# Kernel tuning notes

Measured on AMD Instinct MI355X. Metric: run time of the kernel, lower is better.

## Reference

```python
import jax, jax.numpy as jnp
import numpy as np

D = 1024
H = 16
K = D // H
B = 2
S = 2048

def setup_inputs() -> dict:
    key = jax.random.key(0)
    k1, k2, k3, k4, k5 = jax.random.split(key, 5)
    x = jax.random.normal(k1, (B, S, D), dtype=jnp.float32)
    # nn.Linear(d, 3d): weight [3d, d], bias [3d]
    Wqkv = jax.random.normal(k2, (3 * D, D), dtype=jnp.float32) / np.sqrt(D)
    bqkv = jax.random.normal(k3, (3 * D,), dtype=jnp.float32) * 0.01
    Wproj = jax.random.normal(k4, (D, D), dtype=jnp.float32) / np.sqrt(D)
    bproj = jax.random.normal(k5, (D,), dtype=jnp.float32) * 0.01
    return {"x": x, "Wqkv": Wqkv, "bqkv": bqkv, "Wproj": Wproj, "bproj": bproj}

def reference(x, Wqkv, bqkv, Wproj, bproj):
    Bsz, Slen, d = x.shape
    # fused QKV projection: [B,S,3d] -> [B,S,3,H,K] -> (3, B, H, S, K)
    qkv = (jnp.einsum('bsd,ed->bse', x, Wqkv) + bqkv).reshape(Bsz, Slen, 3, H, K)
    q, k, v = jnp.moveaxis(qkv, 2, 0).transpose(0, 1, 3, 2, 4)
    scale = 1.0 / jnp.sqrt(jnp.asarray(K, dtype=x.dtype))
    scores = jnp.einsum('bhqk,bhmk->bhqm', q, k) * scale  # [B,H,S,S]
    a = jax.nn.softmax(scores, axis=-1)
    # dropout is identity in eval mode
    o = jnp.einsum('bhqm,bhmk->bhqk', a, v)  # [B,H,S,K]
    o = o.transpose(0, 2, 1, 3).reshape(Bsz, Slen, d)
    return jnp.einsum('bsd,ed->bse', o, Wproj) + bproj
```

## Files before the change

kernel.cpp:

```cpp
#include <hip/hip_runtime.h>
#include <cstdint>

typedef unsigned short ushort_t;
typedef short short8 __attribute__((ext_vector_type(8)));
typedef float f32x4 __attribute__((ext_vector_type(4)));
typedef float float4v __attribute__((ext_vector_type(4)));
typedef unsigned int uint2v __attribute__((ext_vector_type(2)));

#define DDIM 1024
#define HH 16
#define HEADK 64
#define BB 2
#define SS 2048

#if __has_builtin(__builtin_amdgcn_exp2f)
#define EXP2F(x) __builtin_amdgcn_exp2f(x)
#else
#define EXP2F(x) exp2f(x)
#endif

__device__ __forceinline__ ushort_t f2bf(float f) {
  union { float f; uint32_t u; } c; c.f = f;
  uint32_t u = c.u;
  u += 0x7fffu + ((u >> 16) & 1u);
  return (ushort_t)(u >> 16);
}

__device__ __forceinline__ uint32_t pkbf_trunc(float a, float b) {
  union { float f; uint32_t u; } ca, cb;
  ca.f = a; cb.f = b;
  return __builtin_amdgcn_perm(cb.u, ca.u, 0x07060302);
}

__device__ __forceinline__ uint32_t pkbf_rne(float a, float b) {
  return (uint32_t)f2bf(a) | ((uint32_t)f2bf(b) << 16);
}

__device__ __forceinline__ void glds16(const ushort_t* gp, ushort_t* lp) {
  __builtin_amdgcn_global_load_lds(
      (const __attribute__((address_space(1))) uint32_t*)gp,
      (__attribute__((address_space(3))) uint32_t*)lp, 16, 0, 0);
}

__global__ void cvt3_kernel(const float* __restrict__ s0, ushort_t* __restrict__ d0, int n0,
                            const float* __restrict__ s1, ushort_t* __restrict__ d1, int n1,
                            const float* __restrict__ s2, ushort_t* __restrict__ d2, int n2) {
  int i = blockIdx.x * blockDim.x + threadIdx.x;
  const float* src; ushort_t* dst; int k;
  if (i < n0) { src = s0; dst = d0; k = i; }
  else if (i < n0 + n1) { src = s1; dst = d1; k = i - n0; }
  else if (i < n0 + n1 + n2) { src = s2; dst = d2; k = i - n0 - n1; }
  else return;
  float4v v = ((const float4v*)src)[k];
  uint2v o; o[0] = pkbf_rne(v[0], v[1]); o[1] = pkbf_rne(v[2], v[3]);
  ((uint2v*)dst)[k] = o;
}

template <int MODE, int TM>
__global__ __launch_bounds__(256) void gemm_nt(
    const ushort_t* __restrict__ A, const ushort_t* __restrict__ Bm,
    const float* __restrict__ bias, float* __restrict__ Cout,
    ushort_t* __restrict__ Cbf, int M, int N, int Kd) {
  __shared__ ushort_t smem[128 * 64 * 2];
  ushort_t* As = smem;
  ushort_t* Bs = smem + TM * 64;
  const int MI = TM / 32;
  const int tid = threadIdx.x;
  const int wv = tid >> 6, lane = tid & 63;
  const int l15 = lane & 15, quad = lane >> 4;
  const int wm = wv >> 1, wn = wv & 1;
  const int tm0 = blockIdx.y * TM, tn0 = blockIdx.x * 128;

  f32x4 acc[MI][4];
#pragma unroll
  for (int i = 0; i < MI; ++i)
#pragma unroll
    for (int j = 0; j < 4; ++j) acc[i][j] = (f32x4){0.f, 0.f, 0.f, 0.f};

  const int lrow = lane >> 3;
  const int gcb = (lane & 7) ^ lrow;
  const int ACI = TM / 32;

  for (int k0 = 0; k0 < Kd; k0 += 64) {
#pragma unroll
    for (int c = 0; c < ACI; ++c) {
      int seg = wv * ACI + c;
      glds16(A + (size_t)(tm0 + seg * 8 + lrow) * Kd + k0 + gcb * 8,
             As + seg * 512);
    }
#pragma unroll
    for (int c = 0; c < 4; ++c) {
      int seg = wv * 4 + c;
      glds16(Bm + (size_t)(tn0 + seg * 8 + lrow) * Kd + k0 + gcb * 8,
             Bs + seg * 512);
    }
    __syncthreads();
#pragma unroll
    for (int kk = 0; kk < 64; kk += 32) {
      short8 af[MI], bfr[4];
#pragma unroll
      for (int i = 0; i < MI; ++i) {
        int r = wm * (TM / 2) + i * 16 + l15;
        int cb = (kk >> 3) + quad;
        af[i] = *(const short8*)(As + r * 64 + ((cb ^ (l15 & 7)) << 3));
      }
#pragma unroll
      for (int j = 0; j < 4; ++j) {
        int r = wn * 64 + j * 16 + l15;
        int cb = (kk >> 3) + quad;
        bfr[j] = *(const short8*)(Bs + r * 64 + ((cb ^ (l15 & 7)) << 3));
      }
#pragma unroll
      for (int i = 0; i < MI; ++i)
#pragma unroll
        for (int j = 0; j < 4; ++j)
          acc[i][j] = __builtin_amdgcn_mfma_f32_16x16x32_bf16(
              af[i], bfr[j], acc[i][j], 0, 0, 0);
    }
    __syncthreads();
  }

  if (MODE == 1) {
#pragma unroll
    for (int j = 0; j < 4; ++j) {
      int col = tn0 + wn * 64 + j * 16 + l15;
      float bv = bias[col];
#pragma unroll
      for (int i = 0; i < MI; ++i) {
        int row0 = tm0 + wm * (TM / 2) + i * 16 + quad * 4;
#pragma unroll
        for (int r = 0; r < 4; ++r)
          Cout[(size_t)(row0 + r) * N + col] = acc[i][j][r] + bv;
      }
    }
  } else {
    const int t = tn0 >> 10;
    if (t < 2) {
#pragma unroll
      for (int j = 0; j < 4; ++j) {
        int col = tn0 + wn * 64 + j * 16 + l15;
        float bv = bias[col];
        int hh = (col >> 6) & 15, kk2 = col & 63;
#pragma unroll
        for (int i = 0; i < MI; ++i) {
          int row0 = tm0 + wm * (TM / 2) + i * 16 + quad * 4;
#pragma unroll
          for (int r = 0; r < 4; ++r) {
            int row = row0 + r;
            int b = row >> 11, s = row & 2047;
            float v = acc[i][j][r] + bv;
            if (t == 0) v *= 0.18033688f;
            size_t base =
                (((size_t)t * BB + b) * HH + hh) * ((size_t)SS * HEADK);
            Cbf[base + (size_t)s * HEADK + kk2] = f2bf(v);
          }
        }
      }
    } else {
      __syncthreads();
#pragma unroll
      for (int j = 0; j < 4; ++j) {
        int c = wn * 64 + j * 16 + l15;
        float bv = bias[tn0 + c];
#pragma unroll
        for (int i = 0; i < MI; ++i) {
          int row0 = wm * (TM / 2) + i * 16 + quad * 4;
          uint2v dw;
          dw[0] = pkbf_rne(acc[i][j][0] + bv, acc[i][j][1] + bv);
          dw[1] = pkbf_rne(acc[i][j][2] + bv, acc[i][j][3] + bv);
          int rb = row0 >> 3;
          *(uint2v*)(&smem[c * 128 + (((rb ^ (c & 15)) << 3) | (row0 & 7))]) =
              dw;
        }
      }
      __syncthreads();
      const int rb2 = lane & 15;
      const int cg = lane >> 4;
#pragma unroll
      for (int it = 0; it < 8; ++it) {
        int c = wv * 32 + it * 4 + cg;
        short8 vv = *(const short8*)(&smem[c * 128 + ((rb2 ^ (c & 15)) << 3)]);
        int gcol = tn0 + c;
        int hh = (gcol >> 6) & 15, kk2 = gcol & 63;
        int grow = tm0 + rb2 * 8;
        int b = grow >> 11, s = grow & 2047;
        size_t base = (((size_t)2 * BB + b) * HH + hh) * ((size_t)SS * HEADK);
        *(short8*)(&Cbf[base + (size_t)kk2 * SS + s]) = vv;
      }
    }
  }
}

__global__ __launch_bounds__(256, 2) void attn_kernel(
    const ushort_t* __restrict__ qkv, ushort_t* __restrict__ ob) {
  __shared__ ushort_t Kt[2][64 * 64];
  __shared__ ushort_t Vt[2][64 * 64];
  __shared__ ushort_t Pw[4][32 * 64];

  const int qt = blockIdx.x, h = blockIdx.y, b = blockIdx.z;
  const int tid = threadIdx.x;
  const int wv = tid >> 6, lane = tid & 63;
  const int l15 = lane & 15, quad = lane >> 4;

  const size_t hstride = (size_t)SS * HEADK;
  const ushort_t* Qg = qkv + ((size_t)(0 * BB + b) * HH + h) * hstride;
  const ushort_t* Kg = qkv + ((size_t)(1 * BB + b) * HH + h) * hstride;
  const ushort_t* Vg = qkv + ((size_t)(2 * BB + b) * HH + h) * hstride;

  short8 qf[2][2];
#pragma unroll
  for (int mi = 0; mi < 2; ++mi)
#pragma unroll
    for (int kc = 0; kc < 2; ++kc)
      qf[mi][kc] = *(const short8*)(
          Qg + (size_t)(qt * 128 + wv * 32 + mi * 16 + l15) * 64 + kc * 32 +
          quad * 8);

  const short ONE = (short)0x3F80;
  short8 ones = {ONE, ONE, ONE, ONE, ONE, ONE, ONE, ONE};

  f32x4 oat[2][4];
  f32x4 loa[2];
#pragma unroll
  for (int mi = 0; mi < 2; ++mi) {
    loa[mi] = (f32x4){0.f, 0.f, 0.f, 0.f};
#pragma unroll
    for (int c = 0; c < 4; ++c) oat[mi][c] = (f32x4){0.f, 0.f, 0.f, 0.f};
  }

  const int lrow = lane >> 3, gcb = (lane & 7) ^ lrow;

  auto stage = [&](int jj, int db) {
#pragma unroll
    for (int c = 0; c < 2; ++c) {
      int seg = wv * 2 + c;
      glds16(Kg + (size_t)(jj * 64 + seg * 8 + lrow) * 64 + gcb * 8,
             &Kt[db][seg * 512]);
    }
#pragma unroll
    for (int c = 0; c < 2; ++c) {
      int seg = wv * 2 + c;
      glds16(Vg + (size_t)(seg * 8 + lrow) * SS + jj * 64 + gcb * 8,
             &Vt[db][seg * 512]);
    }
  };

  stage(0, 0);

  for (int j = 0; j < 32; ++j) {
    const int db = j & 1;
    __syncthreads();
    if (j + 1 < 32) stage(j + 1, db ^ 1);

    f32x4 st[2][4];
#pragma unroll
    for (int cf = 0; cf < 4; ++cf) {
      int n = cf * 16 + l15;
      short8 kf0 = *(const short8*)(&Kt[db][n * 64 + ((quad ^ (n & 7)) << 3)]);
      short8 kf1 =
          *(const short8*)(&Kt[db][n * 64 + (((quad + 4) ^ (n & 7)) << 3)]);
#pragma unroll
      for (int mi = 0; mi < 2; ++mi) {
        f32x4 z = (f32x4){0.f, 0.f, 0.f, 0.f};
        z = __builtin_amdgcn_mfma_f32_16x16x32_bf16(kf0, qf[mi][0], z, 0, 0, 0);
        z = __builtin_amdgcn_mfma_f32_16x16x32_bf16(kf1, qf[mi][1], z, 0, 0, 0);
        st[mi][cf] = z;
      }
    }

#pragma unroll
    for (int mi = 0; mi < 2; ++mi)
#pragma unroll
      for (int cf = 0; cf < 4; ++cf) {
        float e0 = EXP2F(st[mi][cf][0]);
        float e1 = EXP2F(st[mi][cf][1]);
        float e2 = EXP2F(st[mi][cf][2]);
        float e3 = EXP2F(st[mi][cf][3]);
        uint2v dw;
        dw[0] = pkbf_trunc(e0, e1);
        dw[1] = pkbf_trunc(e2, e3);
        int row = mi * 16 + l15;
        int bb = 2 * cf + (quad >> 1);
        *(uint2v*)(&Pw[wv][row * 64 + ((bb ^ (l15 & 7)) << 3) +
                           (quad & 1) * 4]) = dw;
      }

    short8 pa[2][2];
#pragma unroll
    for (int mi = 0; mi < 2; ++mi)
#pragma unroll
      for (int kc = 0; kc < 2; ++kc)
        pa[mi][kc] = *(const short8*)(&Pw[wv][(mi * 16 + l15) * 64 +
                                              (((kc * 4 + quad) ^ (l15 & 7))
                                               << 3)]);

#pragma unroll
    for (int cf = 0; cf < 4; ++cf) {
      int f = cf * 16 + l15;
      short8 vb0 = *(const short8*)(&Vt[db][f * 64 + ((quad ^ (f & 7)) << 3)]);
      short8 vb1 =
          *(const short8*)(&Vt[db][f * 64 + (((quad + 4) ^ (f & 7)) << 3)]);
#pragma unroll
      for (int mi = 0; mi < 2; ++mi) {
        oat[mi][cf] = __builtin_amdgcn_mfma_f32_16x16x32_bf16(
            vb0, pa[mi][0], oat[mi][cf], 0, 0, 0);
        oat[mi][cf] = __builtin_amdgcn_mfma_f32_16x16x32_bf16(
            vb1, pa[mi][1], oat[mi][cf], 0, 0, 0);
      }
    }
#pragma unroll
    for (int mi = 0; mi < 2; ++mi) {
      loa[mi] = __builtin_amdgcn_mfma_f32_16x16x32_bf16(ones, pa[mi][0],
                                                        loa[mi], 0, 0, 0);
      loa[mi] = __builtin_amdgcn_mfma_f32_16x16x32_bf16(ones, pa[mi][1],
                                                        loa[mi], 0, 0, 0);
    }
  }

#pragma unroll
  for (int mi = 0; mi < 2; ++mi) {
    float inv = 1.0f / loa[mi][0];
#pragma unroll
    for (int cf = 0; cf < 4; ++cf) {
      uint2v dw;
      dw[0] = pkbf_rne(oat[mi][cf][0] * inv, oat[mi][cf][1] * inv);
      dw[1] = pkbf_rne(oat[mi][cf][2] * inv, oat[mi][cf][3] * inv);
      int row = mi * 16 + l15;
      int bb = 2 * cf + (quad >> 1);
      *(uint2v*)(&Pw[wv][row * 64 + ((bb ^ (l15 & 7)) << 3) + (quad & 1) * 4]) =
          dw;
    }
  }
  const int rr = lane >> 1, half = lane & 1;
#pragma unroll
  for (int c = 0; c < 4; ++c) {
    short8 ov = *(const short8*)(&Pw[wv][rr * 64 +
                                         (((half * 4 + c) ^ (rr & 7)) << 3)]);
    int row = qt * 128 + wv * 32 + rr;
    *(short8*)(&ob[(size_t)(b * SS + row) * DDIM + h * 64 + half * 32 +
                   c * 8]) = ov;
  }
}

extern "C" void kernel_launch(void* const* d_in, const int* in_sizes, int n_in,
                              void* d_out, int out_size, void* d_ws,
                              size_t ws_size, hipStream_t stream) {
  const float* x = (const float*)d_in[0];
  const float* Wqkv = (const float*)d_in[1];
  const float* bqkv = (const float*)d_in[2];
  const float* Wproj = (const float*)d_in[3];
  const float* bproj = (const float*)d_in[4];
  float* out = (float*)d_out;

  ushort_t* xb = (ushort_t*)d_ws;
  ushort_t* wqb = xb + (size_t)4096 * 1024;
  ushort_t* wpb = wqb + (size_t)3072 * 1024;
  ushort_t* qkvb = wpb + (size_t)1024 * 1024;
  ushort_t* obuf = qkvb + (size_t)3 * BB * HH * SS * HEADK;

  const int n0 = 4096 * 1024 / 4, n1 = 3072 * 1024 / 4, n2 = 1024 * 1024 / 4;
  cvt3_kernel<<<(n0 + n1 + n2 + 255) / 256, 256, 0, stream>>>(
      x, xb, n0, Wqkv, wqb, n1, Wproj, wpb, n2);
  gemm_nt<0, 128><<<dim3(3072 / 128, 4096 / 128), 256, 0, stream>>>(
      xb, wqb, bqkv, nullptr, qkvb, 4096, 3072, 1024);
  attn_kernel<<<dim3(SS / 128, HH, BB), 256, 0, stream>>>(qkvb, obuf);
  gemm_nt<1, 64><<<dim3(1024 / 128, 4096 / 64), 256, 0, stream>>>(
      obuf, wpb, bproj, out, nullptr, 4096, 1024, 1024);
}
```

Baseline: 193.1 us.

## Split attention over key halves with partial outputs and a reduce kernel

The attention kernel now splits the key sequence into two halves, each block processing 32-key tiles for one half. Unnormalized partial outputs (bf16) and partial row sums are written to aliased workspace buffers. A new reduce kernel sums the halves, normalizes, and writes the head-interleaved output. This doubles the block count and raises occupancy to increase parallelism across CUs, at the cost of extra global traffic, an extra launch, and an added bf16 rounding of the partials.

```diff
diff --git a/kernel.cpp b/kernel.cpp
--- a/kernel.cpp
+++ b/kernel.cpp
@@ -34,6 +34,13 @@
 
 __device__ __forceinline__ uint32_t pkbf_rne(float a, float b) {
   return (uint32_t)f2bf(a) | ((uint32_t)f2bf(b) << 16);
+}
+
+__device__ __forceinline__ float bfhi2f(uint32_t u) {
+  union { uint32_t u; float f; } c; c.u = u & 0xffff0000u; return c.f;
+}
+__device__ __forceinline__ float bflo2f(uint32_t u) {
+  union { uint32_t u; float f; } c; c.u = u << 16; return c.f;
 }
 
 __device__ __forceinline__ void glds16(const ushort_t* gp, ushort_t* lp) {
@@ -191,13 +198,15 @@
   }
 }
 
-__global__ __launch_bounds__(256, 2) void attn_kernel(
-    const ushort_t* __restrict__ qkv, ushort_t* __restrict__ ob) {
-  __shared__ ushort_t Kt[2][64 * 64];
-  __shared__ ushort_t Vt[2][64 * 64];
-  __shared__ ushort_t Pw[4][32 * 64];
-
-  const int qt = blockIdx.x, h = blockIdx.y, b = blockIdx.z;
+__global__ __launch_bounds__(256, 4) void attn_kernel(
+    const ushort_t* __restrict__ qkv, ushort_t* __restrict__ Op0,
+    ushort_t* __restrict__ Op1, float* __restrict__ Lp) {
+  __shared__ ushort_t Kt[2][32 * 64];
+  __shared__ ushort_t Vt[2][64 * 32];
+  __shared__ ushort_t Pw[4][32 * 32];
+
+  const int qt = blockIdx.x, h = blockIdx.y;
+  const int b = blockIdx.z >> 1, ns = blockIdx.z & 1;
   const int tid = threadIdx.x;
   const int wv = tid >> 6, lane = tid & 63;
   const int l15 = lane & 15, quad = lane >> 4;
@@ -206,6 +215,7 @@
   const ushort_t* Qg = qkv + ((size_t)(0 * BB + b) * HH + h) * hstride;
   const ushort_t* Kg = qkv + ((size_t)(1 * BB + b) * HH + h) * hstride;
   const ushort_t* Vg = qkv + ((size_t)(2 * BB + b) * HH + h) * hstride;
+  ushort_t* Opp = ns ? Op1 : Op0;
 
   short8 qf[2][2];
 #pragma unroll
@@ -229,20 +239,16 @@
   }
 
   const int lrow = lane >> 3, gcb = (lane & 7) ^ lrow;
+  const int vfl = lane >> 2;
+  const int vgb = (lane & 3) ^ ((vfl >> 1) & 3);
+
+  const int pos0 = ns * (SS / 2);
 
   auto stage = [&](int jj, int db) {
-#pragma unroll
-    for (int c = 0; c < 2; ++c) {
-      int seg = wv * 2 + c;
-      glds16(Kg + (size_t)(jj * 64 + seg * 8 + lrow) * 64 + gcb * 8,
-             &Kt[db][seg * 512]);
-    }
-#pragma unroll
-    for (int c = 0; c < 2; ++c) {
-      int seg = wv * 2 + c;
-      glds16(Vg + (size_t)(seg * 8 + lrow) * SS + jj * 64 + gcb * 8,
-             &Vt[db][seg * 512]);
-    }
+    glds16(Kg + (size_t)(pos0 + jj * 32 + wv * 8 + lrow) * 64 + gcb * 8,
+           &Kt[db][wv * 512]);
+    glds16(Vg + (size_t)(wv * 16 + vfl) * SS + pos0 + jj * 32 + vgb * 8,
+           &Vt[db][wv * 512]);
   };
 
   stage(0, 0);
@@ -252,9 +258,9 @@
     __syncthreads();
     if (j + 1 < 32) stage(j + 1, db ^ 1);
 
-    f32x4 st[2][4];
-#pragma unroll
-    for (int cf = 0; cf < 4; ++cf) {
+    f32x4 st[2][2];
+#pragma unroll
+    for (int cf = 0; cf < 2; ++cf) {
       int n = cf * 16 + l15;
       short8 kf0 = *(const short8*)(&Kt[db][n * 64 + ((quad ^ (n & 7)) << 3)]);
       short8 kf1 =
@@ -271,7 +277,7 @@
 #pragma unroll
     for (int mi = 0; mi < 2; ++mi)
 #pragma unroll
-      for (int cf = 0; cf < 4; ++cf) {
+      for (int cf = 0; cf < 2; ++cf) {
         float e0 = EXP2F(st[mi][cf][0]);
         float e1 = EXP2F(st[mi][cf][1]);
         float e2 = EXP2F(st[mi][cf][2]);
@@ -280,66 +286,90 @@
         dw[0] = pkbf_trunc(e0, e1);
         dw[1] = pkbf_trunc(e2, e3);
         int row = mi * 16 + l15;
-        int bb = 2 * cf + (quad >> 1);
-        *(uint2v*)(&Pw[wv][row * 64 + ((bb ^ (l15 & 7)) << 3) +
-                           (quad & 1) * 4]) = dw;
-      }
-
-    short8 pa[2][2];
+        int pb = 2 * cf + (quad >> 1);
+        int pbs = pb ^ ((l15 >> 1) & 3);
+        *(uint2v*)(&Pw[wv][row * 32 + pbs * 8 + (quad & 1) * 4]) = dw;
+      }
+
+    short8 pa[2];
+#pragma unroll
+    for (int mi = 0; mi < 2; ++mi) {
+      int row = mi * 16 + l15;
+      pa[mi] = *(const short8*)(&Pw[wv][row * 32 +
+                                        ((quad ^ ((l15 >> 1) & 3)) << 3)]);
+    }
+
+#pragma unroll
+    for (int cf = 0; cf < 4; ++cf) {
+      short8 vf = *(const short8*)(&Vt[db][(cf * 16 + l15) * 32 +
+                                           ((quad ^ ((l15 >> 1) & 3)) << 3)]);
+#pragma unroll
+      for (int mi = 0; mi < 2; ++mi)
+        oat[mi][cf] = __builtin_amdgcn_mfma_f32_16x16x32_bf16(
+            vf, pa[mi], oat[mi][cf], 0, 0, 0);
+    }
 #pragma unroll
     for (int mi = 0; mi < 2; ++mi)
-#pragma unroll
-      for (int kc = 0; kc < 2; ++kc)
-        pa[mi][kc] = *(const short8*)(&Pw[wv][(mi * 16 + l15) * 64 +
-                                              (((kc * 4 + quad) ^ (l15 & 7))
-                                               << 3)]);
-
-#pragma unroll
-    for (int cf = 0; cf < 4; ++cf) {
-      int f = cf * 16 + l15;
-      short8 vb0 = *(const short8*)(&Vt[db][f * 64 + ((quad ^ (f & 7)) << 3)]);
-      short8 vb1 =
-          *(const short8*)(&Vt[db][f * 64 + (((quad + 4) ^ (f & 7)) << 3)]);
-#pragma unroll
-      for (int mi = 0; mi < 2; ++mi) {
-        oat[mi][cf] = __builtin_amdgcn_mfma_f32_16x16x32_bf16(
-            vb0, pa[mi][0], oat[mi][cf], 0, 0, 0);
-        oat[mi][cf] = __builtin_amdgcn_mfma_f32_16x16x32_bf16(
-            vb1, pa[mi][1], oat[mi][cf], 0, 0, 0);
-      }
-    }
-#pragma unroll
-    for (int mi = 0; mi < 2; ++mi) {
-      loa[mi] = __builtin_amdgcn_mfma_f32_16x16x32_bf16(ones, pa[mi][0],
-                                                        loa[mi], 0, 0, 0);
-      loa[mi] = __builtin_amdgcn_mfma_f32_16x16x32_bf16(ones, pa[mi][1],
-                                                        loa[mi], 0, 0, 0);
-    }
+      loa[mi] = __builtin_amdgcn_mfma_f32_16x16x32_bf16(ones, pa[mi], loa[mi],
+                                                        0, 0, 0);
   }
 
+  const size_t obase = ((size_t)b * HH + h) * SS * HEADK;
 #pragma unroll
   for (int mi = 0; mi < 2; ++mi) {
-    float inv = 1.0f / loa[mi][0];
 #pragma unroll
     for (int cf = 0; cf < 4; ++cf) {
       uint2v dw;
-      dw[0] = pkbf_rne(oat[mi][cf][0] * inv, oat[mi][cf][1] * inv);
-      dw[1] = pkbf_rne(oat[mi][cf][2] * inv, oat[mi][cf][3] * inv);
-      int row = mi * 16 + l15;
-      int bb = 2 * cf + (quad >> 1);
-      *(uint2v*)(&Pw[wv][row * 64 + ((bb ^ (l15 & 7)) << 3) + (quad & 1) * 4]) =
-          dw;
+      dw[0] = pkbf_rne(oat[mi][cf][0], oat[mi][cf][1]);
+      dw[1] = pkbf_rne(oat[mi][cf][2], oat[mi][cf][3]);
+      int cb = 2 * cf + (quad >> 1);
+      int cbs = cb ^ (l15 & 7);
+      *(uint2v*)(&Pw[wv][l15 * 64 + cbs * 8 + (quad & 1) * 4]) = dw;
+    }
+    const int r = lane >> 2;
+#pragma unroll
+    for (int pass = 0; pass < 2; ++pass) {
+      int g = (lane & 3) + 4 * pass;
+      short8 ov = *(const short8*)(&Pw[wv][r * 64 + ((g ^ (r & 7)) << 3)]);
+      int qrow = qt * 128 + wv * 32 + mi * 16 + r;
+      *(short8*)(&Opp[obase + (size_t)qrow * 64 + g * 8]) = ov;
+    }
+    if (quad == 0) {
+      int qrow = qt * 128 + wv * 32 + mi * 16 + l15;
+      Lp[((size_t)(ns * BB + b) * HH + h) * SS + qrow] = loa[mi][0];
     }
   }
-  const int rr = lane >> 1, half = lane & 1;
-#pragma unroll
-  for (int c = 0; c < 4; ++c) {
-    short8 ov = *(const short8*)(&Pw[wv][rr * 64 +
-                                         (((half * 4 + c) ^ (rr & 7)) << 3)]);
-    int row = qt * 128 + wv * 32 + rr;
-    *(short8*)(&ob[(size_t)(b * SS + row) * DDIM + h * 64 + half * 32 +
-                   c * 8]) = ov;
-  }
+}
+
+__global__ void reduce_kernel(const ushort_t* __restrict__ Op0,
+                              const ushort_t* __restrict__ Op1,
+                              const float* __restrict__ Lp,
+                              ushort_t* __restrict__ ob) {
+  const size_t nsL = (size_t)BB * HH * SS;
+  int c = blockIdx.x * blockDim.x + threadIdx.x;
+  int fc = c & 7;
+  int hh = (c >> 3) & 15;
+  int row = c >> 7;
+  int b = row >> 11, s = row & 2047;
+  size_t po = (((size_t)b * HH + hh) * SS + s) * 64 + fc * 8;
+  uint2v a0 = *(const uint2v*)(&Op0[po]);
+  uint2v a1 = *(const uint2v*)(&Op0[po + 4]);
+  uint2v b0 = *(const uint2v*)(&Op1[po]);
+  uint2v b1 = *(const uint2v*)(&Op1[po + 4]);
+  size_t lo = ((size_t)b * HH + hh) * SS + s;
+  float inv = 1.0f / (Lp[lo] + Lp[nsL + lo]);
+  uint2v o0, o1;
+  o0[0] = pkbf_rne((bflo2f(a0[0]) + bflo2f(b0[0])) * inv,
+                   (bfhi2f(a0[0]) + bfhi2f(b0[0])) * inv);
+  o0[1] = pkbf_rne((bflo2f(a0[1]) + bflo2f(b0[1])) * inv,
+                   (bfhi2f(a0[1]) + bfhi2f(b0[1])) * inv);
+  o1[0] = pkbf_rne((bflo2f(a1[0]) + bflo2f(b1[0])) * inv,
+                   (bfhi2f(a1[0]) + bfhi2f(b1[0])) * inv);
+  o1[1] = pkbf_rne((bflo2f(a1[1]) + bflo2f(b1[1])) * inv,
+                   (bfhi2f(a1[1]) + bfhi2f(b1[1])) * inv);
+  size_t oo = ((size_t)(b * SS + s)) * DDIM + hh * 64 + fc * 8;
+  *(uint2v*)(&ob[oo]) = o0;
+  *(uint2v*)(&ob[oo + 4]) = o1;
 }
 
 extern "C" void kernel_launch(void* const* d_in, const int* in_sizes, int n_in,
@@ -356,14 +386,19 @@
   ushort_t* wqb = xb + (size_t)4096 * 1024;
   ushort_t* wpb = wqb + (size_t)3072 * 1024;
   ushort_t* qkvb = wpb + (size_t)1024 * 1024;
-  ushort_t* obuf = qkvb + (size_t)3 * BB * HH * SS * HEADK;
+  ushort_t* Op1 = qkvb + (size_t)3 * BB * HH * SS * HEADK;
+  ushort_t* Op0 = xb;
+  float* Lp = (float*)wqb;
+  ushort_t* obuf = qkvb;
 
   const int n0 = 4096 * 1024 / 4, n1 = 3072 * 1024 / 4, n2 = 1024 * 1024 / 4;
   cvt3_kernel<<<(n0 + n1 + n2 + 255) / 256, 256, 0, stream>>>(
       x, xb, n0, Wqkv, wqb, n1, Wproj, wpb, n2);
   gemm_nt<0, 128><<<dim3(3072 / 128, 4096 / 128), 256, 0, stream>>>(
       xb, wqb, bqkv, nullptr, qkvb, 4096, 3072, 1024);
-  attn_kernel<<<dim3(SS / 128, HH, BB), 256, 0, stream>>>(qkvb, obuf);
+  attn_kernel<<<dim3(16, 16, 4), 256, 0, stream>>>(qkvb, Op0, Op1, Lp);
+  reduce_kernel<<<(BB * SS * DDIM / 8) / 256, 256, 0, stream>>>(Op0, Op1, Lp,
+                                                                obuf);
   gemm_nt<1, 64><<<dim3(1024 / 128, 4096 / 64), 256, 0, stream>>>(
       obuf, wpb, bproj, out, nullptr, 4096, 1024, 1024);
 }
```

Result: no change. 192.8 us (-0.2%).
